# Performance work log

Measured on AMD Instinct MI355X. Metric: run time of the kernel, lower is better.

## Reference

```python
import jax, jax.numpy as jnp
import numpy as np


def setup_inputs() -> dict:
    key = jax.random.key(0)
    k1, k2, k3 = jax.random.split(key, 3)
    B, C, O, NF = 4, 16, 16, 9  # num_flows fixed at 9 (3x3 stencil)
    x = jax.random.normal(k1, (B, C, 450, 480), dtype=jnp.float32)
    combinator = jax.random.normal(k2, (O, C * NF), dtype=jnp.float32) * 0.05
    bias = jax.random.normal(k3, (O,), dtype=jnp.float32) * 0.05
    return {"x": x, "combinator": combinator, "bias": bias}


def reference(x, combinator, bias):
    # Original forward: zero-pad x by 1, gather the 9 shifted copies
    # (dy,dx) in row-major order over {-1,0,1}^2, flatten (flow, channel)
    # flow-major, then matmul with combinator and add bias.
    # out[b,o,h,w] = sum_{i,c} combinator[o, i*C + c] * x[b,c,h+dy_i,w+dx_i]
    # with flow index i = (dy+1)*3 + (dx+1) = ky*3 + kx, this is exactly a
    # 3x3 cross-correlation (padding=1) with weight[o,c,ky,kx] =
    # combinator[o, (ky*3+kx)*C + c].
    O = combinator.shape[0]
    C = x.shape[1]
    w = combinator.reshape(O, 3, 3, C).transpose(0, 3, 1, 2)  # OIHW
    out = jax.lax.conv_general_dilated(
        x, w,
        window_strides=(1, 1),
        padding=((1, 1), (1, 1)),
        dimension_numbers=("NCHW", "OIHW", "NCHW"),
    )
    return out + bias[None, :, None, None]
```

## Files before the change

### kernel.cpp

```cpp
#include <hip/hip_runtime.h>


#define HH 450
#define WW 480
#define BB 4
#define CC 16
#define OO 16
#define WT    96
#define WQN   5
#define WIN   104
#define RSTG  20
#define ROUT  18
#define HG    25
#define NTILE 6
#define W4N   26
#define HALF  (RSTG * W4N)
#define ITEMS (2 * HALF)
#define PLANE (RSTG * WIN)
#define NBLK  (BB * WQN * HG)

typedef __attribute__((ext_vector_type(8))) short    bf16x8;
typedef __attribute__((ext_vector_type(4))) float    f32x4;
typedef __attribute__((ext_vector_type(4))) unsigned u32x4;

static __device__ __forceinline__ unsigned cvt_pk_bf16(float a, float b) {
    unsigned r;
    asm("v_cvt_pk_bf16_f32 %0, %1, %2" : "=v"(r) : "v"(a), "v"(b));
    return r;
}

__global__ __launch_bounds__(256, 2) void flow_mfma_kernel(
    const float* __restrict__ x, const float* __restrict__ comb,
    const float* __restrict__ bias, float* __restrict__ out)
{
    __shared__ __align__(16) short xs[2 * PLANE][8];

    const int tid  = threadIdx.x;
    const int lane = tid & 63;
    const int wv   = tid >> 6;

    int bid = blockIdx.x;
    int xcd = bid & 7, pos = bid >> 3;
    int L   = (xcd < 4) ? xcd * 63 + pos : 4 * 63 + (xcd - 4) * 62 + pos;
    int hg  = L % HG;
    int t2  = L / HG;
    int wq  = t2 % WQN;
    int b   = t2 / WQN;
    int h0  = hg * ROUT;
    int w0  = wq * WT;

    const int col = lane & 15;
    const int grp = lane >> 4;
    bf16x8 af[5];
    #pragma unroll
    for (int m = 0; m < 5; ++m) {
        int k0 = m * 32 + grp * 8;
        u32x4 p;
        if (k0 < 144) {
            float4 u = *(const float4*)(comb + col * 144 + k0);
            float4 v = *(const float4*)(comb + col * 144 + k0 + 4);
            p[0] = cvt_pk_bf16(u.x, u.y);
            p[1] = cvt_pk_bf16(u.z, u.w);
            p[2] = cvt_pk_bf16(v.x, v.y);
            p[3] = cvt_pk_bf16(v.z, v.w);
        } else {
            p[0] = p[1] = p[2] = p[3] = 0u;
        }
        af[m] = __builtin_bit_cast(bf16x8, p);
    }
    f32x4 bv = *(const f32x4*)(bias + grp * 4);

    auto stage = [&](int s) {
        int cs  = (s >= HALF) ? 1 : 0;
        int rem = s - cs * HALF;
        int r   = rem / W4N;
        int wi4 = rem - r * W4N;
        int hy  = h0 - 1 + r;
        int w   = w0 - 4 + wi4 * 4;
        u32x4 p[4];
        if (((unsigned)hy < (unsigned)HH) && ((unsigned)w < (unsigned)WW)) {
            const float* xp = x + (((size_t)(b * CC + cs * 8) * HH + hy) * WW + w);
            float4 v[8];
            #pragma unroll
            for (int j = 0; j < 8; ++j)
                v[j] = *(const float4*)(xp + (size_t)j * HH * WW);
            #pragma unroll
            for (int q = 0; q < 4; ++q) {
                p[0][q] = cvt_pk_bf16(v[2*q].x, v[2*q+1].x);
                p[1][q] = cvt_pk_bf16(v[2*q].y, v[2*q+1].y);
                p[2][q] = cvt_pk_bf16(v[2*q].z, v[2*q+1].z);
                p[3][q] = cvt_pk_bf16(v[2*q].w, v[2*q+1].w);
            }
        } else {
            #pragma unroll
            for (int k = 0; k < 4; ++k)
                p[k][0] = p[k][1] = p[k][2] = p[k][3] = 0u;
        }
        int r2 = cs * PLANE + r * WIN + wi4 * 4;
        #pragma unroll
        for (int k = 0; k < 4; ++k)
            *(u32x4*)(&xs[r2 + k][0]) = p[k];
    };
    #pragma unroll
    for (int it = 0; it < 4; ++it)
        stage(tid + it * 256);
    if (tid < ITEMS - 4 * 256)
        stage(tid + 4 * 256);
    __syncthreads();

    const int fo = grp >> 1;
    const int ch = grp & 1;
    int cof[5];
    #pragma unroll
    for (int m = 0; m < 4; ++m) {
        int i  = 2 * m + fo;
        int ky = i / 3;
        int kx = i - ky * 3;
        cof[m] = ch * PLANE + ky * WIN + col + kx + 3;
    }
    cof[4] = ch * PLANE + 2 * WIN + col + 5;

    #pragma unroll
    for (int k = 0; k < 27; ++k) {
        int idx = wv + 4 * k;
        int row = idx / 6;
        int t   = idx - row * 6;
        int h   = h0 + row;
        int n0  = t * 16;
        int rbase = row * WIN + n0;
        f32x4 acc = bv;
        #pragma unroll
        for (int m = 0; m < 4; ++m) {
            bf16x8 bf = *(const bf16x8*)(&xs[rbase + cof[m]][0]);
            acc = __builtin_amdgcn_mfma_f32_16x16x32_bf16(af[m], bf, acc, 0, 0, 0);
        }
        bf16x8 b4;
        if (grp < 2) {
            b4 = *(const bf16x8*)(&xs[rbase + cof[4]][0]);
        } else {
            #pragma unroll
            for (int j = 0; j < 8; ++j) b4[j] = 0;
        }
        acc = __builtin_amdgcn_mfma_f32_16x16x32_bf16(af[4], b4, acc, 0, 0, 0);

        float* op = out + (((size_t)(b * OO + grp * 4) * HH + h) * WW + w0 + n0 + col);
        #pragma unroll
        for (int j = 0; j < 4; ++j)
            op[(size_t)j * HH * WW] = acc[j];
    }
}

extern "C" void kernel_launch(void* const* d_in, const int* in_sizes, int n_in,
                              void* d_out, int out_size, void* d_ws, size_t ws_size,
                              hipStream_t stream) {
    const float* x    = (const float*)d_in[0];
    const float* comb = (const float*)d_in[1];
    const float* bias = (const float*)d_in[2];
    float* out        = (float*)d_out;

    flow_mfma_kernel<<<NBLK, 256, 0, stream>>>(x, comb, bias, out);
}
```

Baseline: 26.04 us.

## Shrink row tiles, raise occupancy, and swap MFMA operands for vectorized stores

Cuts output rows per block from 18 to 12 (38 row groups, 760 blocks) and raises launch bounds to 3 blocks per SM, giving more parallelism and a smaller LDS footprint per block. A bounds check skips rows past the image end, since 38*12 exceeds 450. The MFMA operands are swapped so each lane holds 4 consecutive output pixels for one output channel, letting results go out as a single float4 store instead of 4 strided scalar stores. The block-to-XCD mapping is simplified for the new block count. The tradeoff is more halo rows re-staged per output row (14 staged for 12 output, versus 20 for 18).

```diff
diff --git a/kernel.cpp b/kernel.cpp
--- a/kernel.cpp
+++ b/kernel.cpp
@@ -9,9 +9,9 @@
 #define WT    96
 #define WQN   5
 #define WIN   104
-#define RSTG  20
-#define ROUT  18
-#define HG    25
+#define RSTG  14
+#define ROUT  12
+#define HG    38
 #define NTILE 6
 #define W4N   26
 #define HALF  (RSTG * W4N)
@@ -29,7 +29,7 @@
     return r;
 }
 
-__global__ __launch_bounds__(256, 2) void flow_mfma_kernel(
+__global__ __launch_bounds__(256, 3) void flow_mfma_kernel(
     const float* __restrict__ x, const float* __restrict__ comb,
     const float* __restrict__ bias, float* __restrict__ out)
 {
@@ -40,8 +40,7 @@
     const int wv   = tid >> 6;
 
     int bid = blockIdx.x;
-    int xcd = bid & 7, pos = bid >> 3;
-    int L   = (xcd < 4) ? xcd * 63 + pos : 4 * 63 + (xcd - 4) * 62 + pos;
+    int L   = (bid & 7) * 95 + (bid >> 3);
     int hg  = L % HG;
     int t2  = L / HG;
     int wq  = t2 % WQN;
@@ -51,7 +50,7 @@
 
     const int col = lane & 15;
     const int grp = lane >> 4;
-    bf16x8 af[5];
+    bf16x8 wf[5];
     #pragma unroll
     for (int m = 0; m < 5; ++m) {
         int k0 = m * 32 + grp * 8;
@@ -66,9 +65,10 @@
         } else {
             p[0] = p[1] = p[2] = p[3] = 0u;
         }
-        af[m] = __builtin_bit_cast(bf16x8, p);
+        wf[m] = __builtin_bit_cast(bf16x8, p);
     }
-    f32x4 bv = *(const f32x4*)(bias + grp * 4);
+    float bcol = bias[col];
+    f32x4 bv = { bcol, bcol, bcol, bcol };
 
     auto stage = [&](int s) {
         int cs  = (s >= HALF) ? 1 : 0;
@@ -102,10 +102,10 @@
             *(u32x4*)(&xs[r2 + k][0]) = p[k];
     };
     #pragma unroll
-    for (int it = 0; it < 4; ++it)
+    for (int it = 0; it < 2; ++it)
         stage(tid + it * 256);
-    if (tid < ITEMS - 4 * 256)
-        stage(tid + 4 * 256);
+    if (tid < ITEMS - 2 * 256)
+        stage(tid + 2 * 256);
     __syncthreads();
 
     const int fo = grp >> 1;
@@ -121,32 +121,32 @@
     cof[4] = ch * PLANE + 2 * WIN + col + 5;
 
     #pragma unroll
-    for (int k = 0; k < 27; ++k) {
+    for (int k = 0; k < 18; ++k) {
         int idx = wv + 4 * k;
         int row = idx / 6;
         int t   = idx - row * 6;
         int h   = h0 + row;
+        if (h >= HH) continue;
         int n0  = t * 16;
         int rbase = row * WIN + n0;
         f32x4 acc = bv;
         #pragma unroll
         for (int m = 0; m < 4; ++m) {
-            bf16x8 bf = *(const bf16x8*)(&xs[rbase + cof[m]][0]);
-            acc = __builtin_amdgcn_mfma_f32_16x16x32_bf16(af[m], bf, acc, 0, 0, 0);
+            bf16x8 xf = *(const bf16x8*)(&xs[rbase + cof[m]][0]);
+            acc = __builtin_amdgcn_mfma_f32_16x16x32_bf16(xf, wf[m], acc, 0, 0, 0);
         }
-        bf16x8 b4;
+        bf16x8 x4;
         if (grp < 2) {
-            b4 = *(const bf16x8*)(&xs[rbase + cof[4]][0]);
+            x4 = *(const bf16x8*)(&xs[rbase + cof[4]][0]);
         } else {
             #pragma unroll
-            for (int j = 0; j < 8; ++j) b4[j] = 0;
+            for (int j = 0; j < 8; ++j) x4[j] = 0;
         }
-        acc = __builtin_amdgcn_mfma_f32_16x16x32_bf16(af[4], b4, acc, 0, 0, 0);
+        acc = __builtin_amdgcn_mfma_f32_16x16x32_bf16(x4, wf[4], acc, 0, 0, 0);
 
-        float* op = out + (((size_t)(b * OO + grp * 4) * HH + h) * WW + w0 + n0 + col);
-        #pragma unroll
-        for (int j = 0; j < 4; ++j)
-            op[(size_t)j * HH * WW] = acc[j];
+        float* op = out + (((size_t)(b * OO + col) * HH + h) * WW
+                           + w0 + n0 + grp * 4);
+        *(f32x4*)op = acc;
     }
 }
 
```

New measurement: 26.23 us. No clear change (+0.7%).
